# Optimization experiments

Measured on AMD Instinct MI355X. Metric: run time of the kernel, lower is better.

The kernel has to match this reference:

```python
import jax, jax.numpy as jnp
import numpy as np

FA, FB_CAT, FM, HID = 133, 147, 8, 100  # atom feat, bond feat (concat), mol feat, hidden
N_ATOMS, N_BONDS, N_MOLS, MAX_NB = 250000, 500000, 10000, 6
DEPTH = 3


def setup_inputs() -> dict:
    key = jax.random.key(0)
    ks = jax.random.split(key, 10)
    f_atoms = jax.random.normal(ks[0], (N_ATOMS, FA), jnp.float32)
    f_bonds = jax.random.normal(ks[1], (N_BONDS, FB_CAT), jnp.float32)
    f_mol = jax.random.normal(ks[2], (N_MOLS, FM), jnp.float32)
    a2b = jax.random.randint(ks[3], (N_ATOMS, MAX_NB), 0, N_BONDS, jnp.int32)
    b2a = jax.random.randint(ks[4], (N_BONDS,), 0, N_ATOMS, jnp.int32)
    b2revb = jax.random.randint(ks[5], (N_BONDS,), 0, N_BONDS, jnp.int32)
    # contiguous molecules of 25 atoms each -> equivalent of ascope segments
    mol_id = (jnp.arange(N_ATOMS, dtype=jnp.int32) // (N_ATOMS // N_MOLS))
    # parameters (Linear with bias=False): stored as (in, out)
    W_i = jax.random.normal(ks[6], (FB_CAT, HID), jnp.float32) * 0.05
    W_h = jax.random.normal(ks[7], (HID, HID), jnp.float32) * 0.05
    W_o = jax.random.normal(ks[8], (HID + FA, HID), jnp.float32) * 0.05
    return {"f_atoms": f_atoms, "f_bonds": f_bonds, "f_mol": f_mol,
            "W_i": W_i, "W_h": W_h, "W_o": W_o,
            "a2b": a2b, "b2a": b2a, "b2revb": b2revb,
            "mol_id": mol_id, "n_mols": N_MOLS}


def reference(f_atoms, f_bonds, f_mol, W_i, W_h, W_o, a2b, b2a, b2revb, mol_id, n_mols):
    act = jax.nn.relu
    inp = act(f_bonds @ W_i)              # (B, H)
    message = inp
    for _ in range(DEPTH - 1):
        nei = message[a2b]                # (A, MAX_NB, H) gather
        a_message = nei.sum(axis=1)       # (A, H)
        message = a_message[b2a] - message[b2revb]  # (B, H)
        message = act(inp + message @ W_h)
        # dropout p=0 (eval) -> identity
    # readout to atoms
    a_message = message[a2b].sum(axis=1)  # (A, H)
    a_input = jnp.concatenate([f_atoms, a_message], axis=1)  # (A, FA+H)
    atom_hiddens = act(a_input @ W_o)     # (A, H)
    # per-molecule mean over ragged segments (ascope equivalent)
    mol_sum = jax.ops.segment_sum(atom_hiddens, mol_id, num_segments=n_mols)
    counts = jax.ops.segment_sum(jnp.ones((atom_hiddens.shape[0],), atom_hiddens.dtype),
                                 mol_id, num_segments=n_mols)
    mol_vecs = mol_sum / jnp.maximum(counts, 1.0)[:, None]  # zero-vec for empty mols
    mol_vecs = jnp.concatenate([mol_vecs, f_mol], axis=1)   # (M, H+FM)
    return mol_vecs, atom_hiddens
```

## Files before the change

kernel.cpp:

```cpp
#include <hip/hip_runtime.h>

#define THREADS 256
#define MS 128

typedef __bf16 bf16x8 __attribute__((ext_vector_type(8)));
typedef float f32x4 __attribute__((ext_vector_type(4)));
typedef float f32x4u __attribute__((ext_vector_type(4), aligned(4)));
typedef unsigned int u32x4 __attribute__((ext_vector_type(4)));

__device__ __forceinline__ unsigned short f2b(float x) {
    unsigned int u = __float_as_uint(x);
    u = (u + 0x7FFFu + ((u >> 16) & 1u)) >> 16;
    return (unsigned short)u;
}
__device__ __forceinline__ float b2f(unsigned short h) {
    return __uint_as_float(((unsigned int)h) << 16);
}
__device__ __forceinline__ bf16x8 as_bf(uint4 q) {
    union { uint4 q; bf16x8 v; } u; u.q = q; return u.v;
}
__device__ __forceinline__ f32x4u nt4(const float* p) {
    return __builtin_nontemporal_load((const f32x4u*)p);
}
__device__ __forceinline__ uint4 ntq(const unsigned short* p) {
    u32x4 v = __builtin_nontemporal_load((const u32x4*)p);
    return make_uint4(v.x, v.y, v.z, v.w);
}

__device__ __forceinline__ void pack_body(const float* __restrict__ W,
                                          unsigned short* __restrict__ out,
                                          int K, int bid, int l)
{
    int kc = bid / 7, nt = bid - kc * 7;
    int k0 = kc * 32 + (l >> 4) * 8;
    int n = nt * 16 + (l & 15);
    unsigned short v[8];
    #pragma unroll
    for (int j = 0; j < 8; ++j) {
        int k = k0 + j;
        float x = (k < K && n < 100) ? W[(size_t)k * 100 + n] : 0.f;
        v[j] = f2b(x);
    }
    *(uint4*)&out[((size_t)bid * 64 + l) * 8] = *(uint4*)v;
}

__device__ __forceinline__ void pack_wo_body(const float* __restrict__ W,
                                             unsigned short* __restrict__ out,
                                             int bid, int l)
{
    int kc = bid / 7, nt = bid - kc * 7;
    int k0 = kc * 32 + (l >> 4) * 8;
    int n = nt * 16 + (l & 15);
    unsigned short v[8];
    #pragma unroll
    for (int j = 0; j < 8; ++j) {
        int k = k0 + j;
        float x = 0.f;
        if (n < 100) {
            if (k < 100)                  x = W[(size_t)(133 + k) * 100 + n];
            else if (k >= 112 && k < 245) x = W[(size_t)(k - 112) * 100 + n];
        }
        v[j] = f2b(x);
    }
    *(uint4*)&out[((size_t)bid * 64 + l) * 8] = *(uint4*)v;
}

__global__ __launch_bounds__(64) void prep(
    const float* __restrict__ Wi, const float* __restrict__ Wh, const float* __restrict__ Wo,
    unsigned short* __restrict__ wfi, unsigned short* __restrict__ wfh,
    unsigned short* __restrict__ wfo, float* __restrict__ out_mol, int nmol_floats)
{
    int bid = blockIdx.x;
    int l = threadIdx.x;
    if (bid < 35) {
        pack_body(Wi, wfi, 147, bid, l);
    } else if (bid < 63) {
        pack_body(Wh, wfh, 100, bid - 35, l);
    } else if (bid < 119) {
        pack_wo_body(Wo, wfo, bid - 63, l);
    } else {
        int idx = (bid - 119) * 64 + l;
        int stride = (gridDim.x - 119) * 64;
        for (int i = idx; i * 4 < nmol_floats; i += stride)
            *(f32x4*)&out_mol[(size_t)i * 4] = (f32x4){0.f, 0.f, 0.f, 0.f};
    }
}

__global__ __launch_bounds__(THREADS) void gather_sum_bf16(
    const unsigned short* __restrict__ msg, const int* __restrict__ a2b,
    unsigned short* __restrict__ amsg, int A)
{
    int t = blockIdx.x * THREADS + threadIdx.x;
    if (t >= A * 16) return;
    int a = t >> 4;
    int c = t & 15;
    if (c >= 14) {
        *(uint4*)&amsg[(size_t)a * MS + c * 8] = make_uint4(0u, 0u, 0u, 0u);
        return;
    }
    const int* nb = a2b + (size_t)a * 6;
    float s[8];
    #pragma unroll
    for (int e = 0; e < 8; ++e) s[e] = 0.f;
    #pragma unroll
    for (int j = 0; j < 6; ++j) {
        uint4 v = *(const uint4*)&msg[(size_t)nb[j] * MS + c * 8];
        const unsigned short* pv = (const unsigned short*)&v;
        #pragma unroll
        for (int e = 0; e < 8; ++e) s[e] += b2f(pv[e]);
    }
    unsigned short r[8];
    #pragma unroll
    for (int e = 0; e < 8; ++e) r[e] = f2b(s[e]);
    *(uint4*)&amsg[(size_t)a * MS + c * 8] = *(uint4*)r;
}

__global__ __launch_bounds__(THREADS) void gemm_in(
    const float* __restrict__ fb, const unsigned short* __restrict__ wf,
    unsigned short* __restrict__ Y, int M)
{
    __shared__ unsigned short Os[64 * 136];
    const int tid = threadIdx.x;
    const int l = tid & 63, w = tid >> 6;
    const int quad = l >> 4, c15 = l & 15;
    const int row0 = blockIdx.x * 64;
    const int rc = min(row0 + w * 16 + c15, M - 1);
    const float* rowp = fb + (size_t)rc * 147;

    uint4 af[5];
    #pragma unroll
    for (int kc = 0; kc < 4; ++kc) {
        f32x4u x0 = nt4(rowp + kc * 32 + quad * 8);
        f32x4u x1 = nt4(rowp + kc * 32 + quad * 8 + 4);
        unsigned short t[8];
        #pragma unroll
        for (int e = 0; e < 4; ++e) { t[e] = f2b(x0[e]); t[4 + e] = f2b(x1[e]); }
        af[kc] = *(uint4*)t;
    }
    {
        unsigned short t[8];
        #pragma unroll
        for (int j = 0; j < 8; ++j) {
            int k = 128 + quad * 8 + j;
            t[j] = (k < 147) ? f2b(__builtin_nontemporal_load(rowp + k)) : (unsigned short)0;
        }
        af[4] = *(uint4*)t;
    }

    f32x4 acc[7];
    #pragma unroll
    for (int nt = 0; nt < 7; ++nt) acc[nt] = (f32x4){0.f, 0.f, 0.f, 0.f};
    #pragma unroll
    for (int kc = 0; kc < 5; ++kc) {
        #pragma unroll
        for (int nt = 0; nt < 7; ++nt) {
            uint4 bq = *(const uint4*)&wf[((size_t)(kc * 7 + nt) * 64 + l) * 8];
            acc[nt] = __builtin_amdgcn_mfma_f32_16x16x32_bf16(as_bf(af[kc]), as_bf(bq), acc[nt], 0, 0, 0);
        }
    }

    #pragma unroll
    for (int nt = 0; nt < 7; ++nt)
        #pragma unroll
        for (int reg = 0; reg < 4; ++reg)
            Os[(w * 16 + quad * 4 + reg) * 136 + nt * 16 + c15] = f2b(fmaxf(acc[nt][reg], 0.f));
    __syncthreads();

    for (int t = tid; t < 64 * 16; t += THREADS) {
        int rl = t >> 4, c = t & 15;
        int rr = row0 + rl;
        if (rr < M) {
            uint4 o = (c < 14) ? *(const uint4*)&Os[rl * 136 + c * 8]
                               : make_uint4(0u, 0u, 0u, 0u);
            *(uint4*)&Y[(size_t)rr * MS + c * 8] = o;
        }
    }
}

__global__ __launch_bounds__(THREADS) void gemm_msg(
    const unsigned short* __restrict__ amsg, const unsigned short* __restrict__ msg,
    const int* __restrict__ b2a, const int* __restrict__ b2revb,
    const unsigned short* __restrict__ wf, const unsigned short* __restrict__ bias,
    unsigned short* __restrict__ Y, int M, int last)
{
    __shared__ unsigned short Os[64 * 136];
    const int tid = threadIdx.x;
    const int l = tid & 63, w = tid >> 6;
    const int quad = l >> 4, c15 = l & 15;
    const int row0 = blockIdx.x * 64;
    const int rc = min(row0 + w * 16 + c15, M - 1);
    const int iA = b2a[rc], iB = b2revb[rc];
    const unsigned short* pa = amsg + (size_t)iA * MS + quad * 8;
    const unsigned short* pb = msg  + (size_t)iB * MS + quad * 8;

    uint4 a1[4], a2[4];
    #pragma unroll
    for (int kc = 0; kc < 4; ++kc) {
        a1[kc] = *(const uint4*)(pa + kc * 32);
        a2[kc] = *(const uint4*)(pb + kc * 32);
    }

    f32x4 acc1[7], acc2[7];
    #pragma unroll
    for (int nt = 0; nt < 7; ++nt) {
        acc1[nt] = (f32x4){0.f, 0.f, 0.f, 0.f};
        acc2[nt] = (f32x4){0.f, 0.f, 0.f, 0.f};
    }
    #pragma unroll
    for (int kc = 0; kc < 4; ++kc) {
        #pragma unroll
        for (int nt = 0; nt < 7; ++nt) {
            uint4 bq = *(const uint4*)&wf[((size_t)(kc * 7 + nt) * 64 + l) * 8];
            acc1[nt] = __builtin_amdgcn_mfma_f32_16x16x32_bf16(as_bf(a1[kc]), as_bf(bq), acc1[nt], 0, 0, 0);
            acc2[nt] = __builtin_amdgcn_mfma_f32_16x16x32_bf16(as_bf(a2[kc]), as_bf(bq), acc2[nt], 0, 0, 0);
        }
    }

    #pragma unroll
    for (int nt = 0; nt < 7; ++nt)
        #pragma unroll
        for (int reg = 0; reg < 4; ++reg)
            Os[(w * 16 + quad * 4 + reg) * 136 + nt * 16 + c15] = f2b(acc1[nt][reg] - acc2[nt][reg]);
    __syncthreads();

    for (int t = tid; t < 64 * 16; t += THREADS) {
        int rl = t >> 4, c = t & 15;
        int rr = row0 + rl;
        if (rr >= M) continue;
        if (c < 14) {
            uint4 o = *(const uint4*)&Os[rl * 136 + c * 8];
            uint4 bq = last ? ntq(&bias[(size_t)rr * MS + c * 8])
                            : *(const uint4*)&bias[(size_t)rr * MS + c * 8];
            const unsigned short* po = (const unsigned short*)&o;
            const unsigned short* pq = (const unsigned short*)&bq;
            unsigned short res[8];
            #pragma unroll
            for (int e = 0; e < 8; ++e)
                res[e] = f2b(fmaxf(b2f(po[e]) + b2f(pq[e]), 0.f));
            *(uint4*)&Y[(size_t)rr * MS + c * 8] = *(uint4*)res;
        } else if (!last) {
            *(uint4*)&Y[(size_t)rr * MS + c * 8] = make_uint4(0u, 0u, 0u, 0u);
        }
    }
}

__global__ __launch_bounds__(THREADS) void gemm_out(
    const float* __restrict__ fa, const unsigned short* __restrict__ msg,
    const int* __restrict__ a2b, const unsigned short* __restrict__ wf,
    const int* __restrict__ mol_id, float* __restrict__ Y,
    float* __restrict__ out_mol, int M)
{
    constexpr int KS = 264;
    __shared__ char smem[64 * KS * 2];
    __shared__ int mids[64];
    unsigned short* Xs = (unsigned short*)smem;
    float* Os = (float*)smem;

    const int tid = threadIdx.x;
    const int l = tid & 63, w = tid >> 6;
    const int quad = l >> 4, c15 = l & 15;
    const int row0 = blockIdx.x * 64;

    if (tid < 64) {
        int rr = row0 + tid;
        mids[tid] = (rr < M) ? mol_id[rr] : -1;
    }

    for (int t = tid; t < 64 * 33; t += THREADS) {
        int rl = t / 33, c = t - rl * 33;
        int rr = min(row0 + rl, M - 1);
        uint4 o;
        if (c < 14) {
            const int* nb = a2b + (size_t)rr * 6;
            float s[8];
            #pragma unroll
            for (int e = 0; e < 8; ++e) s[e] = 0.f;
            #pragma unroll
            for (int j = 0; j < 6; ++j) {
                uint4 v = *(const uint4*)&msg[(size_t)nb[j] * MS + c * 8];
                const unsigned short* pv = (const unsigned short*)&v;
                #pragma unroll
                for (int e = 0; e < 8; ++e) s[e] += b2f(pv[e]);
            }
            unsigned short r[8];
            #pragma unroll
            for (int e = 0; e < 8; ++e) r[e] = f2b(s[e]);
            o = *(uint4*)r;
        } else if (c < 30) {
            int cc = c - 14;
            f32x4u x0 = nt4(fa + (size_t)rr * 133 + cc * 8);
            f32x4u x1 = nt4(fa + (size_t)rr * 133 + cc * 8 + 4);
            unsigned short tt[8];
            #pragma unroll
            for (int e = 0; e < 4; ++e) { tt[e] = f2b(x0[e]); tt[4 + e] = f2b(x1[e]); }
            o = *(uint4*)tt;
        } else if (c == 30) {
            unsigned short tt[8];
            #pragma unroll
            for (int j = 0; j < 8; ++j) {
                int col = 128 + j;
                tt[j] = (col < 133) ? f2b(__builtin_nontemporal_load(fa + (size_t)rr * 133 + col))
                                    : (unsigned short)0;
            }
            o = *(uint4*)tt;
        } else {
            o = make_uint4(0u, 0u, 0u, 0u);
        }
        *(uint4*)&Xs[(size_t)rl * KS + c * 8] = o;
    }
    __syncthreads();

    f32x4 acc[7];
    #pragma unroll
    for (int nt = 0; nt < 7; ++nt) acc[nt] = (f32x4){0.f, 0.f, 0.f, 0.f};
    const unsigned short* xrow = Xs + (size_t)(w * 16 + c15) * KS + quad * 8;
    #pragma unroll
    for (int kc = 0; kc < 8; ++kc) {
        bf16x8 av = *(const bf16x8*)(xrow + kc * 32);
        #pragma unroll
        for (int nt = 0; nt < 7; ++nt) {
            uint4 bq = *(const uint4*)&wf[((size_t)(kc * 7 + nt) * 64 + l) * 8];
            acc[nt] = __builtin_amdgcn_mfma_f32_16x16x32_bf16(av, as_bf(bq), acc[nt], 0, 0, 0);
        }
    }
    __syncthreads();

    #pragma unroll
    for (int nt = 0; nt < 7; ++nt) {
        int n = nt * 16 + c15;
        if (n < 100) {
            #pragma unroll
            for (int reg = 0; reg < 4; ++reg)
                Os[(w * 16 + quad * 4 + reg) * 108 + n] = fmaxf(acc[nt][reg], 0.f);
        }
    }
    __syncthreads();

    for (int t = tid; t < 64 * 25; t += THREADS) {
        int rl = t / 25, c = t - rl * 25;
        int rr = row0 + rl;
        if (rr < M)
            __builtin_nontemporal_store(*(const f32x4*)&Os[rl * 108 + c * 4],
                                        (f32x4*)&Y[(size_t)rr * 100 + c * 4]);
    }

    if (tid < 100) {
        int c = tid;
        float s = 0.f;
        int cur = mids[0];
        #pragma unroll 1
        for (int rl = 0; rl < 64; ++rl) {
            int mid = mids[rl];
            if (mid != cur) {
                if (cur >= 0) atomicAdd(&out_mol[(size_t)cur * 108 + c], s);
                s = 0.f;
                cur = mid;
            }
            if (mid < 0) break;
            s += Os[rl * 108 + c];
        }
        if (cur >= 0) atomicAdd(&out_mol[(size_t)cur * 108 + c], s);
    }
}

__global__ __launch_bounds__(128) void finalize(
    float* __restrict__ out_mol, const float* __restrict__ f_mol,
    const int* __restrict__ mol_id, int n_atoms)
{
    int m = blockIdx.x;
    int lo = 0, hi = n_atoms;
    while (lo < hi) { int mid = (lo + hi) >> 1; if (mol_id[mid] < m) lo = mid + 1; else hi = mid; }
    int lo2 = lo, hi2 = n_atoms;
    while (lo2 < hi2) { int mid = (lo2 + hi2) >> 1; if (mol_id[mid] < m + 1) lo2 = mid + 1; else hi2 = mid; }
    float inv = 1.0f / fmaxf((float)(lo2 - lo), 1.0f);
    int c = threadIdx.x;
    if (c < 100) {
        out_mol[(size_t)m * 108 + c] *= inv;
    } else if (c < 108) {
        out_mol[(size_t)m * 108 + c] = f_mol[(size_t)m * 8 + (c - 100)];
    }
}

extern "C" void kernel_launch(void* const* d_in, const int* in_sizes, int n_in,
                              void* d_out, int out_size, void* d_ws, size_t ws_size,
                              hipStream_t stream)
{
    const float* f_atoms = (const float*)d_in[0];
    const float* f_bonds = (const float*)d_in[1];
    const float* f_mol   = (const float*)d_in[2];
    const float* W_i     = (const float*)d_in[3];
    const float* W_h     = (const float*)d_in[4];
    const float* W_o     = (const float*)d_in[5];
    const int* a2b    = (const int*)d_in[6];
    const int* b2a    = (const int*)d_in[7];
    const int* b2revb = (const int*)d_in[8];
    const int* mol_id = (const int*)d_in[9];

    const int A    = in_sizes[0] / 133;
    const int B    = in_sizes[1] / 147;
    const int Mmol = in_sizes[2] / 8;

    unsigned short* wsu = (unsigned short*)d_ws;
    unsigned short* wfi  = wsu;
    unsigned short* wfh  = wfi + 35 * 512;
    unsigned short* wfo  = wfh + 28 * 512;
    unsigned short* amsg = wfo + 56 * 512;
    unsigned short* inp  = amsg + (size_t)A * MS;
    unsigned short* msgA = inp  + (size_t)B * MS;
    unsigned short* msgB = msgA + (size_t)B * MS;

    float* out     = (float*)d_out;
    float* out_mol = out;
    float* atom_h  = out + (size_t)Mmol * 108;

    dim3 blk(THREADS);
    int gB = (B + 63) / 64;
    int gA = (A + 63) / 64;
    int gg = (A * 16 + THREADS - 1) / THREADS;

    prep<<<119 + 256, dim3(64), 0, stream>>>(W_i, W_h, W_o, wfi, wfh, wfo,
                                             out_mol, Mmol * 108);

    gemm_in<<<gB, blk, 0, stream>>>(f_bonds, wfi, inp, B);

    gather_sum_bf16<<<gg, blk, 0, stream>>>(inp, a2b, amsg, A);
    gemm_msg<<<gB, blk, 0, stream>>>(amsg, inp, b2a, b2revb, wfh, inp, msgA, B, 0);

    gather_sum_bf16<<<gg, blk, 0, stream>>>(msgA, a2b, amsg, A);
    gemm_msg<<<gB, blk, 0, stream>>>(amsg, msgA, b2a, b2revb, wfh, inp, msgB, B, 1);

    gemm_out<<<gA, blk, 0, stream>>>(f_atoms, msgB, a2b, wfo, mol_id, atom_h, out_mol, A);

    finalize<<<Mmol, dim3(128), 0, stream>>>(out_mol, f_mol, mol_id, A);
}
```

Before: 1.099 ms.

## Stage f_bonds tile through LDS with coalesced loads; drop nontemporal hints

gemm_in now loads the 64-row fp32 f_bonds tile cooperatively into shared memory with row-contiguous 8-float chunks, converts to bf16, then each wave reads MFMA A fragments from LDS, instead of each lane loading strided pieces of its own row directly. All nontemporal load/store builtins are replaced by ordinary loads and stores across gemm_in, the message GEMM and gemm_out. The staging is meant to improve global-memory coalescing of the largest input read, at the cost of an extra LDS round trip and barrier; removing the nontemporal hints changes cache behaviour, which could help or hurt streaming traffic.

```diff
diff --git a/kernel.cpp b/kernel.cpp
--- a/kernel.cpp
+++ b/kernel.cpp
@@ -6,7 +6,6 @@
 typedef __bf16 bf16x8 __attribute__((ext_vector_type(8)));
 typedef float f32x4 __attribute__((ext_vector_type(4)));
 typedef float f32x4u __attribute__((ext_vector_type(4), aligned(4)));
-typedef unsigned int u32x4 __attribute__((ext_vector_type(4)));
 
 __device__ __forceinline__ unsigned short f2b(float x) {
     unsigned int u = __float_as_uint(x);
@@ -18,13 +17,6 @@
 }
 __device__ __forceinline__ bf16x8 as_bf(uint4 q) {
     union { uint4 q; bf16x8 v; } u; u.q = q; return u.v;
-}
-__device__ __forceinline__ f32x4u nt4(const float* p) {
-    return __builtin_nontemporal_load((const f32x4u*)p);
-}
-__device__ __forceinline__ uint4 ntq(const unsigned short* p) {
-    u32x4 v = __builtin_nontemporal_load((const u32x4*)p);
-    return make_uint4(v.x, v.y, v.z, v.w);
 }
 
 __device__ __forceinline__ void pack_body(const float* __restrict__ W,
@@ -119,45 +111,52 @@
     const float* __restrict__ fb, const unsigned short* __restrict__ wf,
     unsigned short* __restrict__ Y, int M)
 {
-    __shared__ unsigned short Os[64 * 136];
+    constexpr int KS = 168;
+    __shared__ char smem[64 * KS * 2];
+    unsigned short* Xs = (unsigned short*)smem;
+    unsigned short* Os = (unsigned short*)smem;
+
     const int tid = threadIdx.x;
     const int l = tid & 63, w = tid >> 6;
     const int quad = l >> 4, c15 = l & 15;
     const int row0 = blockIdx.x * 64;
-    const int rc = min(row0 + w * 16 + c15, M - 1);
-    const float* rowp = fb + (size_t)rc * 147;
-
-    uint4 af[5];
-    #pragma unroll
-    for (int kc = 0; kc < 4; ++kc) {
-        f32x4u x0 = nt4(rowp + kc * 32 + quad * 8);
-        f32x4u x1 = nt4(rowp + kc * 32 + quad * 8 + 4);
-        unsigned short t[8];
-        #pragma unroll
-        for (int e = 0; e < 4; ++e) { t[e] = f2b(x0[e]); t[4 + e] = f2b(x1[e]); }
-        af[kc] = *(uint4*)t;
-    }
-    {
-        unsigned short t[8];
-        #pragma unroll
-        for (int j = 0; j < 8; ++j) {
-            int k = 128 + quad * 8 + j;
-            t[j] = (k < 147) ? f2b(__builtin_nontemporal_load(rowp + k)) : (unsigned short)0;
-        }
-        af[4] = *(uint4*)t;
-    }
+
+    for (int t = tid; t < 64 * 20; t += THREADS) {
+        int rl = t / 20, c = t - rl * 20;
+        int rr = min(row0 + rl, M - 1);
+        const float* rowp = fb + (size_t)rr * 147 + c * 8;
+        unsigned short tt[8];
+        if (c < 18) {
+            f32x4u x0 = *(const f32x4u*)(rowp);
+            f32x4u x1 = *(const f32x4u*)(rowp + 4);
+            #pragma unroll
+            for (int e = 0; e < 4; ++e) { tt[e] = f2b(x0[e]); tt[4 + e] = f2b(x1[e]); }
+        } else if (c == 18) {
+            #pragma unroll
+            for (int j = 0; j < 8; ++j)
+                tt[j] = (j < 3) ? f2b(rowp[j]) : (unsigned short)0;
+        } else {
+            #pragma unroll
+            for (int j = 0; j < 8; ++j) tt[j] = 0;
+        }
+        *(uint4*)&Xs[(size_t)rl * KS + c * 8] = *(uint4*)tt;
+    }
+    __syncthreads();
 
     f32x4 acc[7];
     #pragma unroll
     for (int nt = 0; nt < 7; ++nt) acc[nt] = (f32x4){0.f, 0.f, 0.f, 0.f};
+    const unsigned short* xrow = Xs + (size_t)(w * 16 + c15) * KS + quad * 8;
     #pragma unroll
     for (int kc = 0; kc < 5; ++kc) {
+        bf16x8 av = *(const bf16x8*)(xrow + kc * 32);
         #pragma unroll
         for (int nt = 0; nt < 7; ++nt) {
             uint4 bq = *(const uint4*)&wf[((size_t)(kc * 7 + nt) * 64 + l) * 8];
-            acc[nt] = __builtin_amdgcn_mfma_f32_16x16x32_bf16(as_bf(af[kc]), as_bf(bq), acc[nt], 0, 0, 0);
-        }
-    }
+            acc[nt] = __builtin_amdgcn_mfma_f32_16x16x32_bf16(av, as_bf(bq), acc[nt], 0, 0, 0);
+        }
+    }
+    __syncthreads();
 
     #pragma unroll
     for (int nt = 0; nt < 7; ++nt)
@@ -229,8 +228,7 @@
         if (rr >= M) continue;
         if (c < 14) {
             uint4 o = *(const uint4*)&Os[rl * 136 + c * 8];
-            uint4 bq = last ? ntq(&bias[(size_t)rr * MS + c * 8])
-                            : *(const uint4*)&bias[(size_t)rr * MS + c * 8];
+            uint4 bq = *(const uint4*)&bias[(size_t)rr * MS + c * 8];
             const unsigned short* po = (const unsigned short*)&o;
             const unsigned short* pq = (const unsigned short*)&bq;
             unsigned short res[8];
@@ -288,8 +286,8 @@
             o = *(uint4*)r;
         } else if (c < 30) {
             int cc = c - 14;
-            f32x4u x0 = nt4(fa + (size_t)rr * 133 + cc * 8);
-            f32x4u x1 = nt4(fa + (size_t)rr * 133 + cc * 8 + 4);
+            f32x4u x0 = *(const f32x4u*)(fa + (size_t)rr * 133 + cc * 8);
+            f32x4u x1 = *(const f32x4u*)(fa + (size_t)rr * 133 + cc * 8 + 4);
             unsigned short tt[8];
             #pragma unroll
             for (int e = 0; e < 4; ++e) { tt[e] = f2b(x0[e]); tt[4 + e] = f2b(x1[e]); }
@@ -299,8 +297,7 @@
             #pragma unroll
             for (int j = 0; j < 8; ++j) {
                 int col = 128 + j;
-                tt[j] = (col < 133) ? f2b(__builtin_nontemporal_load(fa + (size_t)rr * 133 + col))
-                                    : (unsigned short)0;
+                tt[j] = (col < 133) ? f2b(fa[(size_t)rr * 133 + col]) : (unsigned short)0;
             }
             o = *(uint4*)tt;
         } else {
@@ -340,8 +337,7 @@
         int rl = t / 25, c = t - rl * 25;
         int rr = row0 + rl;
         if (rr < M)
-            __builtin_nontemporal_store(*(const f32x4*)&Os[rl * 108 + c * 4],
-                                        (f32x4*)&Y[(size_t)rr * 100 + c * 4]);
+            *(f32x4*)&Y[(size_t)rr * 100 + c * 4] = *(const f32x4*)&Os[rl * 108 + c * 4];
     }
 
     if (tid < 100) {
```

Result: faster. 1.039 ms (-5.4%).
